# Optimization experiments

Measured on AMD Instinct MI355X. Metric: run time of the kernel, lower is better.

Reference implementation:

```python
import jax, jax.numpy as jnp
import numpy as np

N, E = 50000, 400000
FN, FE, FG = 32, 16, 16
H1, H2 = 256, 128


def seg_mean(x, idx, n):
    # mean of edge rows per segment; empty segments -> 0 (scatter_mean semantics)
    s = jax.ops.segment_sum(x, idx, num_segments=n)
    c = jax.ops.segment_sum(jnp.ones((x.shape[0], 1), x.dtype), idx, num_segments=n)
    return s / jnp.maximum(c, 1.0)


def setup_inputs() -> dict:
    key = jax.random.key(0)
    ks = jax.random.split(key, 32)
    g = lambda k, shape, s=0.05: jax.random.normal(k, shape, dtype=jnp.float32) * s
    return {
        'nodes': g(ks[0], (N, FN), 1.0),
        'edges': g(ks[1], (E, FE), 1.0),
        'globals_u': g(ks[2], (FG,), 1.0),
        'senders': jax.random.randint(ks[3], (E,), 0, N, dtype=jnp.int32),
        'receivers': jax.random.randint(ks[4], (E,), 0, N, dtype=jnp.int32),
        'We1': g(ks[5], (FE, H1)), 'be1': jnp.zeros((H1,), jnp.float32),
        'Wn1': g(ks[6], (FN, H1)), 'Win1': g(ks[7], (H1, H1)), 'Wout1': g(ks[8], (H1, H1)), 'bn1': jnp.zeros((H1,), jnp.float32),
        'Wu1': g(ks[9], (FG, H1)), 'Wgn1': g(ks[10], (H1, H1)), 'Wge1': g(ks[11], (H1, H1)), 'bu1': jnp.zeros((H1,), jnp.float32),
        'We2': g(ks[12], (H1, H2)), 'be2': jnp.zeros((H2,), jnp.float32),
        'Wn2': g(ks[13], (H1, H2)), 'Win2': g(ks[14], (H2, H2)), 'Wout2': g(ks[15], (H2, H2)), 'bn2': jnp.zeros((H2,), jnp.float32),
        'Wu2': g(ks[16], (H1, H2)), 'Wgn2': g(ks[17], (H2, H2)), 'Wge2': g(ks[18], (H2, H2)), 'bu2': jnp.zeros((H2,), jnp.float32),
    }


def reference(nodes, edges, globals_u, senders, receivers,
              We1, be1, Wn1, Win1, Wout1, bn1, Wu1, Wgn1, Wge1, bu1,
              We2, be2, Wn2, Win2, Wout2, bn2, Wu2, Wgn2, Wge2, bu2):
    n = nodes.shape[0]
    # --- block 1 (width 256) ---
    e1 = jax.nn.relu(edges @ We1 + be1)                                  # [E, H1]
    inc1 = seg_mean(e1, receivers, n)                                    # avg incoming edges per node
    out1 = seg_mean(e1, senders, n)                                      # avg outgoing edges per node
    n1 = jax.nn.relu(nodes @ Wn1 + inc1 @ Win1 + out1 @ Wout1 + bn1)     # [N, H1]
    u1 = jax.nn.relu(globals_u @ Wu1 + n1.mean(0) @ Wgn1 + e1.mean(0) @ Wge1 + bu1)  # [H1]
    # --- block 2 (width 128) ---
    e2 = jax.nn.relu(e1 @ We2 + be2)                                     # [E, H2]
    inc2 = seg_mean(e2, receivers, n)
    out2 = seg_mean(e2, senders, n)
    n2 = jax.nn.relu(n1 @ Wn2 + inc2 @ Win2 + out2 @ Wout2 + bn2)        # [N, H2]
    u2 = jax.nn.relu(u1 @ Wu2 + n2.mean(0) @ Wgn2 + e2.mean(0) @ Wge2 + bu2)  # [H2]
    return n2, e2, u2
```

## Files before the change

kernel.cpp:

```cpp
#include <hip/hip_runtime.h>
#include <hip/hip_bf16.h>
#include <stdint.h>

#define NN 50000
#define NE 400000
#define FN 32
#define FE 16
#define FG 16
#define H1 256
#define H2 128
#define M2 (2*NN)
#define SCAN_B 391
#define NPART 256

typedef unsigned short u16;
typedef __bf16 bfv8 __attribute__((ext_vector_type(8)));
typedef float f32v4 __attribute__((ext_vector_type(4)));
typedef u16 usv2 __attribute__((ext_vector_type(2)));
typedef u16 usv4 __attribute__((ext_vector_type(4)));
typedef u16 usv8 __attribute__((ext_vector_type(8)));

#define APK 264
#define AP2 136
#define EP1 40


__device__ __forceinline__ u16 f2b(float x){
  __hip_bfloat16 h = __float2bfloat16(x);
  return *reinterpret_cast<u16*>(&h);
}
__device__ __forceinline__ float bf2f(u16 u){
  union{uint32_t i; float f;} v; v.i = ((uint32_t)u) << 16; return v.f;
}

template<int NCK, int NNT, int PITCH>
__device__ __forceinline__ void gemm_tiles(const u16* a_s, const u16* __restrict__ pB,
                                           int w, int l, f32v4* acc)
{
  const int lr = l & 15, q = l >> 4;
  const bfv8* bp = (const bfv8*)pB;
  for (int ck = 0; ck < NCK; ck++){
    bfv8 a = *(const bfv8*)&a_s[(w*16 + lr)*PITCH + ck*32 + q*8];
    #pragma unroll
    for (int nt = 0; nt < NNT; nt++){
      bfv8 b = bp[(ck*NNT + nt)*64 + l];
      acc[nt] = __builtin_amdgcn_mfma_f32_16x16x32_bf16(a, b, acc[nt], 0, 0, 0);
    }
  }
}

template<int C4PR_LOG2>
__device__ __forceinline__ void stage_rows(u16* a_s, const float* __restrict__ src,
                                           long n0, int t)
{
  const int c4pr = 1 << C4PR_LOG2;
  for (int idx = t; idx < 64*c4pr; idx += 256){
    int row = idx >> C4PR_LOG2, c4 = idx & (c4pr - 1);
    long n = n0 + row;
    float x0=0.f, x1=0.f, x2=0.f, x3=0.f;
    if (n < NN){
      const float4 v = *(const float4*)&src[(n << (C4PR_LOG2 + 2)) + c4*4];
      x0 = v.x; x1 = v.y; x2 = v.z; x3 = v.w;
    }
    usv4 o; o.x = f2b(x0); o.y = f2b(x1); o.z = f2b(x2); o.w = f2b(x3);
    *(usv4*)&a_s[row*APK + c4*4] = o;
  }
}

struct PD { const float* src; u16* dst; int K, N, Ks, perm; };
struct PackArgs { PD d[8]; };

__global__ __launch_bounds__(64) void pack_weights(PackArgs A){
  int b = blockIdx.x, l = threadIdx.x;
  int mi = 0, base = 0;
  for (; mi < 8; mi++){
    int tiles = (A.d[mi].K >> 5) * (A.d[mi].N >> 4);
    if (b < base + tiles) break;
    base += tiles;
  }
  const PD d = A.d[mi];
  const int tile = b - base;
  const int ntn = d.N >> 4;
  const int ck = tile / ntn, nt = tile % ntn;
  const int lr = l & 15, q = l >> 4;
  const int col = nt*16 + lr;
  usv8 o;
  #pragma unroll
  for (int j = 0; j < 8; j++){
    int k = ck*32 + q*8 + j;
    int sk = (d.perm == 1) ? (((k & 15) << 4) | (k >> 4)) : k;
    o[j] = (k < d.Ks) ? f2b(d.src[(long)sk * d.N + col]) : (u16)0;
  }
  *(usv8*)&d.dst[((long)tile*64 + l)*8] = o;
}

__global__ __launch_bounds__(256) void csr_count(const int* __restrict__ recv,
    const int* __restrict__ send, int* cnt, int* pos_in, int* pos_out)
{
  int e = blockIdx.x*256 + threadIdx.x;
  if (e >= NE) return;
  pos_in [e] = atomicAdd(&cnt[recv[e]], 1);
  pos_out[e] = atomicAdd(&cnt[NN + send[e]], 1);
}

__global__ __launch_bounds__(256) void scan_blocks(const int* __restrict__ cnt,
    int* off, int* btot)
{
  __shared__ int s[256];
  int b = blockIdx.x, t = threadIdx.x;
  int i = b*256 + t;
  int v = (i < M2) ? cnt[i] : 0;
  s[t] = v; __syncthreads();
  int acc = v;
  for (int d = 1; d < 256; d <<= 1){
    int add = (t >= d) ? s[t-d] : 0;
    __syncthreads();
    acc += add; s[t] = acc;
    __syncthreads();
  }
  if (i < M2) off[i] = acc - v;
  if (t == 255) btot[b] = acc;
}

__global__ __launch_bounds__(256) void scan_tops(int* btot){
  __shared__ int s[512], ts[256];
  int t = threadIdx.x;
  s[t]     = (t < SCAN_B) ? btot[t] : 0;
  s[256+t] = (256+t < SCAN_B) ? btot[256+t] : 0;
  __syncthreads();
  int a0 = s[2*t], a1 = s[2*t+1];
  int tot = a0 + a1;
  ts[t] = tot; __syncthreads();
  int acc = tot;
  for (int d = 1; d < 256; d <<= 1){
    int add = (t >= d) ? ts[t-d] : 0;
    __syncthreads();
    acc += add; ts[t] = acc;
    __syncthreads();
  }
  int excl = acc - tot;
  if (2*t   < SCAN_B) btot[2*t]   = excl;
  if (2*t+1 < SCAN_B) btot[2*t+1] = excl + a0;
}

__global__ __launch_bounds__(256) void scan_fix(int* off, const int* __restrict__ btot){
  int i = blockIdx.x*256 + threadIdx.x;
  if (i < M2) off[i] += btot[blockIdx.x];
}

__global__ __launch_bounds__(256) void csr_fill(const int* __restrict__ recv,
    const int* __restrict__ send, const int* __restrict__ off,
    const int* __restrict__ pos_in, const int* __restrict__ pos_out, int* lis)
{
  int e = blockIdx.x*256 + threadIdx.x;
  if (e >= NE) return;
  lis[off[recv[e]]      + pos_in [e]] = e;
  lis[off[NN + send[e]] + pos_out[e]] = e;
}

__global__ __launch_bounds__(256) void edge1_kernel(const float* __restrict__ edges,
    const u16* __restrict__ pWe1, const float* __restrict__ be1,
    u16* __restrict__ e1b, float* __restrict__ e1p)
{
  __shared__ __align__(16) u16 a_es[64*EP1];
  __shared__ float cs_s[H1];
  __shared__ float bs[H1];
  const int t = threadIdx.x;
  const long e0 = (long)blockIdx.x * 64;
  const int w = t >> 6, l = t & 63, lr = l & 15, q = l >> 4;
  cs_s[t] = 0.f;
  bs[t] = be1[t];
  {
    int row = t >> 2, c4 = t & 3;
    float4 v = *(const float4*)&edges[(e0 + row)*FE + c4*4];
    usv4 o = { f2b(v.x), f2b(v.y), f2b(v.z), f2b(v.w) };
    *(usv4*)&a_es[row*EP1 + c4*4] = o;
    *(usv4*)&a_es[row*EP1 + 16 + c4*4] = (usv4){0,0,0,0};
  }
  __syncthreads();
  f32v4 acc[16];
  #pragma unroll
  for (int nt = 0; nt < 16; nt++) acc[nt] = (f32v4){0.f,0.f,0.f,0.f};
  gemm_tiles<1,16,EP1>(a_es, pWe1, w, l, acc);

  #pragma unroll
  for (int nt = 0; nt < 16; nt++){
    const float b = bs[nt*16 + lr];
    float part = 0.f;
    #pragma unroll
    for (int r = 0; r < 4; r++){
      float v = fmaxf(acc[nt][r] + b, 0.f);
      acc[nt][r] = v; part += v;
    }
    part += __shfl_xor(part, 16);
    part += __shfl_xor(part, 32);
    if (q == 0) atomicAdd(&cs_s[nt*16 + lr], part);
  }
  usv8 ob0[4], ob1[4];
  #pragma unroll
  for (int r = 0; r < 4; r++){
    #pragma unroll
    for (int h = 0; h < 8; h++){ ob0[r][h] = f2b(acc[h][r]); ob1[r][h] = f2b(acc[8+h][r]); }
  }
  __syncthreads();
  atomicAdd(&e1p[(blockIdx.x & (NPART-1))*H1 + t], cs_s[t]);
  #pragma unroll
  for (int r = 0; r < 4; r++){
    const int m = w*16 + q*4 + r;
    *(usv8*)&e1b[(e0 + m)*H1 + lr*16]     = ob0[r];
    *(usv8*)&e1b[(e0 + m)*H1 + lr*16 + 8] = ob1[r];
  }
}

__global__ __launch_bounds__(256) void e2_kernel(float* __restrict__ e2f,
    const u16* __restrict__ pWe2, const float* __restrict__ be2, float* __restrict__ e2p)
{
  __shared__ __align__(16) u16 a_s[64*APK];
  __shared__ float cs_s[H2];
  __shared__ float bs[H2];
  const int t = threadIdx.x;
  const long e0 = (long)blockIdx.x * 64;
  const int w = t >> 6, l = t & 63, lr = l & 15, q = l >> 4;
  if (t < H2){ cs_s[t] = 0.f; bs[t] = be2[t]; }
  const u16* e1u = (const u16*)e2f;
  for (int idx = t; idx < 64*32; idx += 256){
    int row = idx >> 5, ch = idx & 31;
    usv8 v = *(const usv8*)&e1u[(e0 + row)*H1 + ch*8];
    *(usv8*)&a_s[row*APK + ch*8] = v;
  }
  __syncthreads();
  f32v4 acc[8];
  #pragma unroll
  for (int nt = 0; nt < 8; nt++) acc[nt] = (f32v4){0.f,0.f,0.f,0.f};
  gemm_tiles<8,8,APK>(a_s, pWe2, w, l, acc);

  #pragma unroll
  for (int nt = 0; nt < 8; nt++){
    const float b = bs[nt*16 + lr];
    float part = 0.f;
    #pragma unroll
    for (int r = 0; r < 4; r++){
      float v = fmaxf(acc[nt][r] + b, 0.f);
      acc[nt][r] = v; part += v;
    }
    part += __shfl_xor(part, 16);
    part += __shfl_xor(part, 32);
    if (q == 0) atomicAdd(&cs_s[nt*16 + lr], part);
  }
  __syncthreads();
  float* fl = (float*)a_s;
  #pragma unroll
  for (int r = 0; r < 4; r++){
    const int m = w*16 + q*4 + r;
    const int sw = (m & 7) * 4;
    #pragma unroll
    for (int nt = 0; nt < 8; nt++)
      fl[m*128 + ((nt*16 + lr) ^ sw)] = acc[nt][r];
  }
  __syncthreads();
  if (t < H2) atomicAdd(&e2p[(blockIdx.x & (NPART-1))*H2 + t], cs_s[t]);
  {
    const int row = t >> 2, c = t & 3;
    const int sw = (row & 7) * 4;
    #pragma unroll
    for (int k = 0; k < 8; k++){
      const int wi = (c*32 + k*4) ^ sw;
      float4 v = *(const float4*)&fl[row*128 + wi];
      *(float4*)&e2f[(e0 + row)*H2 + c*32 + k*4] = v;
    }
  }
}

template<int PITCH>
__device__ __forceinline__ void gather_h1(u16* a_s, const u16* __restrict__ src,
    const int* roff, const int* __restrict__ lis, int w, int l)
{
  for (int rr = 0; rr < 16; rr++){
    int r = w + rr*4;
    int rs = roff[r], re = roff[r+1];
    float s0=0.f, s1=0.f, s2=0.f, s3=0.f;
    int j = rs;
    for (; j + 8 <= re; j += 8){
      int i0=lis[j],i1=lis[j+1],i2=lis[j+2],i3=lis[j+3];
      int i4=lis[j+4],i5=lis[j+5],i6=lis[j+6],i7=lis[j+7];
      usv4 a0 = *(const usv4*)&src[(long)i0*H1 + l*4];
      usv4 a1 = *(const usv4*)&src[(long)i1*H1 + l*4];
      usv4 a2 = *(const usv4*)&src[(long)i2*H1 + l*4];
      usv4 a3 = *(const usv4*)&src[(long)i3*H1 + l*4];
      usv4 a4 = *(const usv4*)&src[(long)i4*H1 + l*4];
      usv4 a5 = *(const usv4*)&src[(long)i5*H1 + l*4];
      usv4 a6 = *(const usv4*)&src[(long)i6*H1 + l*4];
      usv4 a7 = *(const usv4*)&src[(long)i7*H1 + l*4];
      s0 += ((bf2f(a0.x)+bf2f(a1.x)) + (bf2f(a2.x)+bf2f(a3.x)))
          + ((bf2f(a4.x)+bf2f(a5.x)) + (bf2f(a6.x)+bf2f(a7.x)));
      s1 += ((bf2f(a0.y)+bf2f(a1.y)) + (bf2f(a2.y)+bf2f(a3.y)))
          + ((bf2f(a4.y)+bf2f(a5.y)) + (bf2f(a6.y)+bf2f(a7.y)));
      s2 += ((bf2f(a0.z)+bf2f(a1.z)) + (bf2f(a2.z)+bf2f(a3.z)))
          + ((bf2f(a4.z)+bf2f(a5.z)) + (bf2f(a6.z)+bf2f(a7.z)));
      s3 += ((bf2f(a0.w)+bf2f(a1.w)) + (bf2f(a2.w)+bf2f(a3.w)))
          + ((bf2f(a4.w)+bf2f(a5.w)) + (bf2f(a6.w)+bf2f(a7.w)));
    }
    for (; j + 4 <= re; j += 4){
      int i0=lis[j],i1=lis[j+1],i2=lis[j+2],i3=lis[j+3];
      usv4 a0 = *(const usv4*)&src[(long)i0*H1 + l*4];
      usv4 a1 = *(const usv4*)&src[(long)i1*H1 + l*4];
      usv4 a2 = *(const usv4*)&src[(long)i2*H1 + l*4];
      usv4 a3 = *(const usv4*)&src[(long)i3*H1 + l*4];
      s0 += (bf2f(a0.x)+bf2f(a1.x)) + (bf2f(a2.x)+bf2f(a3.x));
      s1 += (bf2f(a0.y)+bf2f(a1.y)) + (bf2f(a2.y)+bf2f(a3.y));
      s2 += (bf2f(a0.z)+bf2f(a1.z)) + (bf2f(a2.z)+bf2f(a3.z));
      s3 += (bf2f(a0.w)+bf2f(a1.w)) + (bf2f(a2.w)+bf2f(a3.w));
    }
    for (; j < re; ++j){
      int i0 = lis[j];
      usv4 a0 = *(const usv4*)&src[(long)i0*H1 + l*4];
      s0 += bf2f(a0.x); s1 += bf2f(a0.y); s2 += bf2f(a0.z); s3 += bf2f(a0.w);
    }
    float rd = 1.f / fmaxf((float)(re - rs), 1.f);
    usv4 o = { f2b(s0*rd), f2b(s1*rd), f2b(s2*rd), f2b(s3*rd) };
    *(usv4*)&a_s[r*PITCH + l*4] = o;
  }
}

template<int PITCH>
__device__ __forceinline__ void gather_h2(u16* a_s, const float* __restrict__ src,
    const int* roff, const int* __restrict__ lis, int w, int l)
{
  for (int rr = 0; rr < 16; rr++){
    int r = w + rr*4;
    int rs = roff[r], re = roff[r+1];
    float s0=0.f, s1=0.f;
    int j = rs;
    for (; j + 8 <= re; j += 8){
      int i0=lis[j],i1=lis[j+1],i2=lis[j+2],i3=lis[j+3];
      int i4=lis[j+4],i5=lis[j+5],i6=lis[j+6],i7=lis[j+7];
      float2 a0 = *(const float2*)&src[(long)i0*H2 + l*2];
      float2 a1 = *(const float2*)&src[(long)i1*H2 + l*2];
      float2 a2 = *(const float2*)&src[(long)i2*H2 + l*2];
      float2 a3 = *(const float2*)&src[(long)i3*H2 + l*2];
      float2 a4 = *(const float2*)&src[(long)i4*H2 + l*2];
      float2 a5 = *(const float2*)&src[(long)i5*H2 + l*2];
      float2 a6 = *(const float2*)&src[(long)i6*H2 + l*2];
      float2 a7 = *(const float2*)&src[(long)i7*H2 + l*2];
      s0 += ((a0.x+a1.x) + (a2.x+a3.x)) + ((a4.x+a5.x) + (a6.x+a7.x));
      s1 += ((a0.y+a1.y) + (a2.y+a3.y)) + ((a4.y+a5.y) + (a6.y+a7.y));
    }
    for (; j + 4 <= re; j += 4){
      int i0=lis[j],i1=lis[j+1],i2=lis[j+2],i3=lis[j+3];
      float2 a0 = *(const float2*)&src[(long)i0*H2 + l*2];
      float2 a1 = *(const float2*)&src[(long)i1*H2 + l*2];
      float2 a2 = *(const float2*)&src[(long)i2*H2 + l*2];
      float2 a3 = *(const float2*)&src[(long)i3*H2 + l*2];
      s0 += (a0.x+a1.x) + (a2.x+a3.x);
      s1 += (a0.y+a1.y) + (a2.y+a3.y);
    }
    for (; j < re; ++j){
      int i0 = lis[j];
      float2 a0 = *(const float2*)&src[(long)i0*H2 + l*2];
      s0 += a0.x; s1 += a0.y;
    }
    float rd = 1.f / fmaxf((float)(re - rs), 1.f);
    usv2 o = { f2b(s0*rd), f2b(s1*rd) };
    *(usv2*)&a_s[r*PITCH + l*2] = o;
  }
}

__global__ __launch_bounds__(256, 4) void node1_kernel(
    const float* __restrict__ nodes, const u16* __restrict__ e1b,
    const int* __restrict__ off, const int* __restrict__ lis,
    const u16* __restrict__ pWn1, const u16* __restrict__ pWin1, const u16* __restrict__ pWout1,
    const float* __restrict__ bn1, u16* __restrict__ n1b, float* __restrict__ n1p)
{
  __shared__ __align__(16) u16 a_s[64*APK];
  __shared__ int roff[65], roff2[65];
  __shared__ float cs_s[H1];
  __shared__ float bs[H1];
  const int t = threadIdx.x;
  const long n0 = (long)blockIdx.x * 64;
  const int w = t >> 6, l = t & 63, lr = l & 15, q = l >> 4;

  cs_s[t] = 0.f;
  bs[t] = bn1[t];
  if (t <= 64){
    long idx = n0 + t;
    roff [t] = (idx >= NN) ? NE     : off[idx];
    roff2[t] = (idx >= NN) ? 2*NE   : off[NN + idx];
  }
  __syncthreads();

  f32v4 acc[16];
  #pragma unroll
  for (int nt = 0; nt < 16; nt++) acc[nt] = (f32v4){0.f,0.f,0.f,0.f};

  gather_h1<APK>(a_s, e1b, roff, lis, w, l);
  __syncthreads();
  gemm_tiles<8,16,APK>(a_s, pWin1, w, l, acc);
  __syncthreads();

  gather_h1<APK>(a_s, e1b, roff2, lis, w, l);
  __syncthreads();
  gemm_tiles<8,16,APK>(a_s, pWout1, w, l, acc);
  __syncthreads();

  stage_rows<3>(a_s, nodes, n0, t);
  __syncthreads();
  gemm_tiles<1,16,APK>(a_s, pWn1, w, l, acc);

  #pragma unroll
  for (int nt = 0; nt < 16; nt++){
    const float b = bs[nt*16 + lr];
    float part = 0.f;
    #pragma unroll
    for (int r = 0; r < 4; r++){
      const long n = n0 + w*16 + q*4 + r;
      float v = fmaxf(acc[nt][r] + b, 0.f);
      acc[nt][r] = v;
      if (n < NN) part += v;
    }
    part += __shfl_xor(part, 16);
    part += __shfl_xor(part, 32);
    if (q == 0) atomicAdd(&cs_s[nt*16 + lr], part);
  }
  __syncthreads();
  atomicAdd(&n1p[(blockIdx.x & (NPART-1))*H1 + t], cs_s[t]);
  #pragma unroll
  for (int r = 0; r < 4; r++){
    const int m = w*16 + q*4 + r;
    const long n = n0 + m;
    if (n < NN){
      usv8 o0, o1;
      #pragma unroll
      for (int h = 0; h < 8; h++){ o0[h] = f2b(acc[h][r]); o1[h] = f2b(acc[8+h][r]); }
      *(usv8*)&n1b[n*H1 + lr*16]     = o0;
      *(usv8*)&n1b[n*H1 + lr*16 + 8] = o1;
    }
  }
}

__global__ __launch_bounds__(256, 4) void node2_kernel(
    const u16* __restrict__ n1b, const float* __restrict__ e2f,
    const int* __restrict__ off, const int* __restrict__ lis,
    const u16* __restrict__ pWn2, const u16* __restrict__ pWin2, const u16* __restrict__ pWout2,
    const float* __restrict__ bn2, float* __restrict__ n2_out, float* __restrict__ n2p)
{
  __shared__ __align__(16) u16 a_s[64*AP2];
  __shared__ int roff[65], roff2[65];
  __shared__ float cs_s[H2];
  const int t = threadIdx.x;
  const long n0 = (long)blockIdx.x * 64;
  const int w = t >> 6, l = t & 63, lr = l & 15, q = l >> 4;

  if (t < H2) cs_s[t] = 0.f;
  if (t <= 64){
    long idx = n0 + t;
    roff [t] = (idx >= NN) ? NE     : off[idx];
    roff2[t] = (idx >= NN) ? 2*NE   : off[NN + idx];
  }
  __syncthreads();

  f32v4 acc[8];
  #pragma unroll
  for (int nt = 0; nt < 8; nt++) acc[nt] = (f32v4){0.f,0.f,0.f,0.f};

  for (int h = 0; h < 2; h++){
    for (int idx = t; idx < 64*16; idx += 256){
      int row = idx >> 4, ch = idx & 15;
      long n = n0 + row;
      usv8 v = (usv8){0,0,0,0,0,0,0,0};
      if (n < NN) v = *(const usv8*)&n1b[n*H1 + h*128 + ch*8];
      *(usv8*)&a_s[row*AP2 + ch*8] = v;
    }
    __syncthreads();
    gemm_tiles<4,8,AP2>(a_s, pWn2 + h*(4*8*64*8), w, l, acc);
    __syncthreads();
  }

  gather_h2<AP2>(a_s, e2f, roff, lis, w, l);
  __syncthreads();
  gemm_tiles<4,8,AP2>(a_s, pWin2, w, l, acc);
  __syncthreads();

  gather_h2<AP2>(a_s, e2f, roff2, lis, w, l);
  __syncthreads();
  gemm_tiles<4,8,AP2>(a_s, pWout2, w, l, acc);

  #pragma unroll
  for (int nt = 0; nt < 8; nt++){
    const float b = bn2[nt*16 + lr];
    float part = 0.f;
    #pragma unroll
    for (int r = 0; r < 4; r++){
      const long n = n0 + w*16 + q*4 + r;
      float v = fmaxf(acc[nt][r] + b, 0.f);
      acc[nt][r] = v;
      if (n < NN) part += v;
    }
    part += __shfl_xor(part, 16);
    part += __shfl_xor(part, 32);
    if (q == 0) atomicAdd(&cs_s[nt*16 + lr], part);
  }
  __syncthreads();
  if (t < H2) atomicAdd(&n2p[(blockIdx.x & (NPART-1))*H2 + t], cs_s[t]);
  #pragma unroll
  for (int nt = 0; nt < 8; nt++){
    const int j = nt*16 + lr;
    #pragma unroll
    for (int r = 0; r < 4; r++){
      const long n = n0 + w*16 + q*4 + r;
      if (n < NN) n2_out[n*H2 + j] = acc[nt][r];
    }
  }
}

__global__ void u1_kernel(const float* __restrict__ gu, const float* __restrict__ Wu1,
    const float* __restrict__ Wgn1, const float* __restrict__ Wge1, const float* __restrict__ bu1,
    const float* __restrict__ n1p, const float* __restrict__ e1p, float* __restrict__ u1v)
{
    __shared__ float ncs[H1], ecs[H1];
    const int j = threadIdx.x;
    float sn = 0.f, se = 0.f;
    #pragma unroll 8
    for (int c = 0; c < NPART; c++){ sn += n1p[c*H1 + j]; se += e1p[c*H1 + j]; }
    ncs[j] = sn; ecs[j] = se;
    __syncthreads();
    float acc = bu1[j];
    #pragma unroll
    for (int k = 0; k < FG; k++) acc += gu[k] * Wu1[k*H1 + j];
    for (int k = 0; k < H1; k++) acc += (ncs[k] * (1.f/NN)) * Wgn1[k*H1 + j];
    for (int k = 0; k < H1; k++) acc += (ecs[k] * (1.f/NE)) * Wge1[k*H1 + j];
    u1v[j] = fmaxf(acc, 0.f);
}

__global__ void u2_kernel(const float* __restrict__ u1v, const float* __restrict__ Wu2,
    const float* __restrict__ Wgn2, const float* __restrict__ Wge2, const float* __restrict__ bu2,
    const float* __restrict__ n2p, const float* __restrict__ e2p, float* __restrict__ u2_out)
{
    __shared__ float ncs[H2], ecs[H2];
    const int j = threadIdx.x;
    float sn = 0.f, se = 0.f;
    #pragma unroll 8
    for (int c = 0; c < NPART; c++){ sn += n2p[c*H2 + j]; se += e2p[c*H2 + j]; }
    ncs[j] = sn; ecs[j] = se;
    __syncthreads();
    float acc = bu2[j];
    for (int k = 0; k < H1; k++) acc += u1v[k] * Wu2[k*H2 + j];
    for (int k = 0; k < H2; k++) acc += (ncs[k] * (1.f/NN)) * Wgn2[k*H2 + j];
    for (int k = 0; k < H2; k++) acc += (ecs[k] * (1.f/NE)) * Wge2[k*H2 + j];
    u2_out[j] = fmaxf(acc, 0.f);
}

extern "C" void kernel_launch(void* const* d_in, const int* in_sizes, int n_in,
                              void* d_out, int out_size, void* d_ws, size_t ws_size,
                              hipStream_t stream)
{
    (void)in_sizes; (void)n_in; (void)out_size; (void)ws_size;
    const float* nodes = (const float*)d_in[0];
    const float* edges = (const float*)d_in[1];
    const float* gu    = (const float*)d_in[2];
    const int* senders   = (const int*)d_in[3];
    const int* receivers = (const int*)d_in[4];
    const float* We1  = (const float*)d_in[5];  const float* be1 = (const float*)d_in[6];
    const float* Wn1  = (const float*)d_in[7];  const float* Win1= (const float*)d_in[8];
    const float* Wout1= (const float*)d_in[9];  const float* bn1 = (const float*)d_in[10];
    const float* Wu1  = (const float*)d_in[11]; const float* Wgn1= (const float*)d_in[12];
    const float* Wge1 = (const float*)d_in[13]; const float* bu1 = (const float*)d_in[14];
    const float* We2  = (const float*)d_in[15]; const float* be2 = (const float*)d_in[16];
    const float* Wn2  = (const float*)d_in[17]; const float* Win2= (const float*)d_in[18];
    const float* Wout2= (const float*)d_in[19]; const float* bn2 = (const float*)d_in[20];
    const float* Wu2  = (const float*)d_in[21]; const float* Wgn2= (const float*)d_in[22];
    const float* Wge2 = (const float*)d_in[23]; const float* bu2 = (const float*)d_in[24];

    float* ws = (float*)d_ws;
    size_t o = 0;
    int*   cnt    = (int*)(ws + o);  o += M2;
    float* e1p    = ws + o;          o += (size_t)NPART*H1;
    float* n1p    = ws + o;          o += (size_t)NPART*H1;
    float* e2p    = ws + o;          o += (size_t)NPART*H2;
    float* n2p    = ws + o;          o += (size_t)NPART*H2;
    const size_t zero_bytes = o * sizeof(float);
    float* u1v    = ws + o;          o += 256;
    int*   off    = (int*)(ws + o);  o += M2;
    int*   pos_in = (int*)(ws + o);  o += NE;
    int*   pos_out= (int*)(ws + o);  o += NE;
    int*   lis    = (int*)(ws + o);  o += 2*NE;
    int*   btot   = (int*)(ws + o);  o += 400;

    u16* pbase = (u16*)(ws + o);
    size_t po = 0;
    u16* pWin1 = pbase + po;  po += (size_t)H1*H1;
    u16* pWout1= pbase + po;  po += (size_t)H1*H1;
    u16* pWn1  = pbase + po;  po += (size_t)FN*H1;
    u16* pWe1  = pbase + po;  po += (size_t)32*H1;
    u16* pWe2  = pbase + po;  po += (size_t)H1*H2;
    u16* pWn2  = pbase + po;  po += (size_t)H1*H2;
    u16* pWin2 = pbase + po;  po += (size_t)H2*H2;
    u16* pWout2= pbase + po;  po += (size_t)H2*H2;
    o += (po + 1) / 2;

    u16* n1b = (u16*)(ws + o);

    float* n2_out = (float*)d_out;
    float* e2f    = n2_out + (size_t)NN*H2;
    float* u2_out = n2_out + (size_t)(NN + NE)*H2;
    u16*   e1b    = (u16*)e2f;

    hipMemsetAsync(d_ws, 0, zero_bytes, stream);

    PackArgs pa;
    pa.d[0] = {Win1,  pWin1,  H1, H1, H1, 1};
    pa.d[1] = {Wout1, pWout1, H1, H1, H1, 1};
    pa.d[2] = {Wn1,   pWn1,   FN, H1, FN, 0};
    pa.d[3] = {We1,   pWe1,   32, H1, FE, 0};
    pa.d[4] = {We2,   pWe2,   H1, H2, H1, 1};
    pa.d[5] = {Wn2,   pWn2,   H1, H2, H1, 1};
    pa.d[6] = {Win2,  pWin2,  H2, H2, H2, 0};
    pa.d[7] = {Wout2, pWout2, H2, H2, H2, 0};
    int total_tiles = 0;
    for (int i = 0; i < 8; i++) total_tiles += (pa.d[i].K >> 5) * (pa.d[i].N >> 4);
    pack_weights<<<total_tiles, 64, 0, stream>>>(pa);

    const int EG = (NE + 255)/256;
    csr_count<<<EG, 256, 0, stream>>>(receivers, senders, cnt, pos_in, pos_out);
    scan_blocks<<<SCAN_B, 256, 0, stream>>>(cnt, off, btot);
    scan_tops<<<1, 256, 0, stream>>>(btot);
    scan_fix<<<SCAN_B, 256, 0, stream>>>(off, btot);
    csr_fill<<<EG, 256, 0, stream>>>(receivers, senders, off, pos_in, pos_out, lis);

    edge1_kernel<<<NE/64, 256, 0, stream>>>(edges, pWe1, be1, e1b, e1p);

    node1_kernel<<<(NN + 63)/64, 256, 0, stream>>>(nodes, e1b, off, lis,
        pWn1, pWin1, pWout1, bn1, n1b, n1p);

    u1_kernel<<<1, H1, 0, stream>>>(gu, Wu1, Wgn1, Wge1, bu1, n1p, e1p, u1v);

    e2_kernel<<<NE/64, 256, 0, stream>>>(e2f, pWe2, be2, e2p);

    node2_kernel<<<(NN + 63)/64, 256, 0, stream>>>(n1b, e2f, off, lis,
        pWn2, pWin2, pWout2, bn2, n2_out, n2p);

    u2_kernel<<<1, H2, 0, stream>>>(u1v, Wu2, Wgn2, Wge2, bu2, n2p, e2p, u2_out);
}
```

Before: 883.0 us.

## Halve node1 row tile and split output columns across warps for occupancy

node1_kernel now processes 32 nodes per block instead of 64. The four warps are arranged 2x2, each covering 16 rows by 8 output tiles, so the accumulator array shrinks from 16 to 8 MFMA tiles and the launch bound rises from 4 to 8 blocks per CU. The aim is more waves in flight to hide the latency of the irregular CSR gathers from e1b. In exchange, each block reads the packed weights for half as many rows, so weight traffic per node doubles, and there are twice as many blocks, each with its own atomic partial-sum update.

```diff
diff --git a/kernel.cpp b/kernel.cpp
--- a/kernel.cpp
+++ b/kernel.cpp
@@ -49,21 +49,19 @@
   }
 }
 
-template<int C4PR_LOG2>
-__device__ __forceinline__ void stage_rows(u16* a_s, const float* __restrict__ src,
-                                           long n0, int t)
-{
-  const int c4pr = 1 << C4PR_LOG2;
-  for (int idx = t; idx < 64*c4pr; idx += 256){
-    int row = idx >> C4PR_LOG2, c4 = idx & (c4pr - 1);
-    long n = n0 + row;
-    float x0=0.f, x1=0.f, x2=0.f, x3=0.f;
-    if (n < NN){
-      const float4 v = *(const float4*)&src[(n << (C4PR_LOG2 + 2)) + c4*4];
-      x0 = v.x; x1 = v.y; x2 = v.z; x3 = v.w;
-    }
-    usv4 o; o.x = f2b(x0); o.y = f2b(x1); o.z = f2b(x2); o.w = f2b(x3);
-    *(usv4*)&a_s[row*APK + c4*4] = o;
+template<int NCK, int NNT_TOT, int NNT, int PITCH>
+__device__ __forceinline__ void gemm_cs(const u16* a_s, const u16* __restrict__ pB,
+                                        int rbase, int ntb, int l, f32v4* acc)
+{
+  const int lr = l & 15, q = l >> 4;
+  const bfv8* bp = (const bfv8*)pB;
+  for (int ck = 0; ck < NCK; ck++){
+    bfv8 a = *(const bfv8*)&a_s[(rbase + lr)*PITCH + ck*32 + q*8];
+    #pragma unroll
+    for (int nt = 0; nt < NNT; nt++){
+      bfv8 b = bp[(ck*NNT_TOT + ntb + nt)*64 + l];
+      acc[nt] = __builtin_amdgcn_mfma_f32_16x16x32_bf16(a, b, acc[nt], 0, 0, 0);
+    }
   }
 }
 
@@ -271,11 +269,10 @@
   }
 }
 
-template<int PITCH>
-__device__ __forceinline__ void gather_h1(u16* a_s, const u16* __restrict__ src,
+__device__ __forceinline__ void gather_h1_32(u16* a_s, const u16* __restrict__ src,
     const int* roff, const int* __restrict__ lis, int w, int l)
 {
-  for (int rr = 0; rr < 16; rr++){
+  for (int rr = 0; rr < 8; rr++){
     int r = w + rr*4;
     int rs = roff[r], re = roff[r+1];
     float s0=0.f, s1=0.f, s2=0.f, s3=0.f;
@@ -318,7 +315,7 @@
     }
     float rd = 1.f / fmaxf((float)(re - rs), 1.f);
     usv4 o = { f2b(s0*rd), f2b(s1*rd), f2b(s2*rd), f2b(s3*rd) };
-    *(usv4*)&a_s[r*PITCH + l*4] = o;
+    *(usv4*)&a_s[r*APK + l*4] = o;
   }
 }
 
@@ -365,74 +362,85 @@
   }
 }
 
-__global__ __launch_bounds__(256, 4) void node1_kernel(
+__global__ __launch_bounds__(256, 8) void node1_kernel(
     const float* __restrict__ nodes, const u16* __restrict__ e1b,
     const int* __restrict__ off, const int* __restrict__ lis,
     const u16* __restrict__ pWn1, const u16* __restrict__ pWin1, const u16* __restrict__ pWout1,
     const float* __restrict__ bn1, u16* __restrict__ n1b, float* __restrict__ n1p)
 {
-  __shared__ __align__(16) u16 a_s[64*APK];
-  __shared__ int roff[65], roff2[65];
+  __shared__ __align__(16) u16 a_s[32*APK];
+  __shared__ int roff[33], roff2[33];
   __shared__ float cs_s[H1];
   __shared__ float bs[H1];
   const int t = threadIdx.x;
-  const long n0 = (long)blockIdx.x * 64;
+  const long n0 = (long)blockIdx.x * 32;
   const int w = t >> 6, l = t & 63, lr = l & 15, q = l >> 4;
+  const int rbase = (w & 1) * 16;
+  const int ntb   = (w >> 1) * 8;
 
   cs_s[t] = 0.f;
   bs[t] = bn1[t];
-  if (t <= 64){
+  if (t <= 32){
     long idx = n0 + t;
     roff [t] = (idx >= NN) ? NE     : off[idx];
     roff2[t] = (idx >= NN) ? 2*NE   : off[NN + idx];
   }
   __syncthreads();
 
-  f32v4 acc[16];
-  #pragma unroll
-  for (int nt = 0; nt < 16; nt++) acc[nt] = (f32v4){0.f,0.f,0.f,0.f};
-
-  gather_h1<APK>(a_s, e1b, roff, lis, w, l);
-  __syncthreads();
-  gemm_tiles<8,16,APK>(a_s, pWin1, w, l, acc);
-  __syncthreads();
-
-  gather_h1<APK>(a_s, e1b, roff2, lis, w, l);
-  __syncthreads();
-  gemm_tiles<8,16,APK>(a_s, pWout1, w, l, acc);
-  __syncthreads();
-
-  stage_rows<3>(a_s, nodes, n0, t);
-  __syncthreads();
-  gemm_tiles<1,16,APK>(a_s, pWn1, w, l, acc);
-
-  #pragma unroll
-  for (int nt = 0; nt < 16; nt++){
-    const float b = bs[nt*16 + lr];
+  f32v4 acc[8];
+  #pragma unroll
+  for (int nt = 0; nt < 8; nt++) acc[nt] = (f32v4){0.f,0.f,0.f,0.f};
+
+  gather_h1_32(a_s, e1b, roff, lis, w, l);
+  __syncthreads();
+  gemm_cs<8,16,8,APK>(a_s, pWin1, rbase, ntb, l, acc);
+  __syncthreads();
+
+  gather_h1_32(a_s, e1b, roff2, lis, w, l);
+  __syncthreads();
+  gemm_cs<8,16,8,APK>(a_s, pWout1, rbase, ntb, l, acc);
+  __syncthreads();
+
+  {
+    int row = t >> 3, c4 = t & 7;
+    long n = n0 + row;
+    float x0=0.f, x1=0.f, x2=0.f, x3=0.f;
+    if (n < NN){
+      const float4 v = *(const float4*)&nodes[n*FN + c4*4];
+      x0 = v.x; x1 = v.y; x2 = v.z; x3 = v.w;
+    }
+    usv4 o; o.x = f2b(x0); o.y = f2b(x1); o.z = f2b(x2); o.w = f2b(x3);
+    *(usv4*)&a_s[row*APK + c4*4] = o;
+  }
+  __syncthreads();
+  gemm_cs<1,16,8,APK>(a_s, pWn1, rbase, ntb, l, acc);
+
+  #pragma unroll
+  for (int nt = 0; nt < 8; nt++){
+    const float b = bs[(ntb + nt)*16 + lr];
     float part = 0.f;
     #pragma unroll
     for (int r = 0; r < 4; r++){
-      const long n = n0 + w*16 + q*4 + r;
+      const long n = n0 + rbase + q*4 + r;
       float v = fmaxf(acc[nt][r] + b, 0.f);
       acc[nt][r] = v;
       if (n < NN) part += v;
     }
     part += __shfl_xor(part, 16);
     part += __shfl_xor(part, 32);
-    if (q == 0) atomicAdd(&cs_s[nt*16 + lr], part);
+    if (q == 0) atomicAdd(&cs_s[(ntb + nt)*16 + lr], part);
   }
   __syncthreads();
   atomicAdd(&n1p[(blockIdx.x & (NPART-1))*H1 + t], cs_s[t]);
   #pragma unroll
   for (int r = 0; r < 4; r++){
-    const int m = w*16 + q*4 + r;
+    const int m = rbase + q*4 + r;
     const long n = n0 + m;
     if (n < NN){
-      usv8 o0, o1;
+      usv8 o0;
       #pragma unroll
-      for (int h = 0; h < 8; h++){ o0[h] = f2b(acc[h][r]); o1[h] = f2b(acc[8+h][r]); }
-      *(usv8*)&n1b[n*H1 + lr*16]     = o0;
-      *(usv8*)&n1b[n*H1 + lr*16 + 8] = o1;
+      for (int h = 0; h < 8; h++) o0[h] = f2b(acc[h][r]);
+      *(usv8*)&n1b[n*H1 + lr*16 + ntb] = o0;
     }
   }
 }
@@ -628,7 +636,7 @@
 
     edge1_kernel<<<NE/64, 256, 0, stream>>>(edges, pWe1, be1, e1b, e1p);
 
-    node1_kernel<<<(NN + 63)/64, 256, 0, stream>>>(nodes, e1b, off, lis,
+    node1_kernel<<<(NN + 31)/32, 256, 0, stream>>>(nodes, e1b, off, lis,
         pWn1, pWin1, pWout1, bn1, n1b, n1p);
 
     u1_kernel<<<1, H1, 0, stream>>>(gu, Wu1, Wgn1, Wge1, bu1, n1p, e1p, u1v);
```

Measured after the change: 1.035 ms. +17.2%, slower.

## Fuse both edge MLP layers into one kernel with e1 kept in workspace

Applied to the files above, without the earlier changes.

Adds an edge kernel that computes e1 = relu(edges@We1+b) and then immediately e2 = relu(e1@We2+b) from LDS. e1 now goes to a separate bf16 workspace buffer rather than aliasing the e2 output region. This removes the separate e2 pass that re-read e1 from global memory. It depends on workspace size being large enough, otherwise it falls back to the old path. It also needs more LDS per block, which may reduce occupancy.

```diff
diff --git a/kernel.cpp b/kernel.cpp
--- a/kernel.cpp
+++ b/kernel.cpp
@@ -156,6 +156,108 @@
   if (e >= NE) return;
   lis[off[recv[e]]      + pos_in [e]] = e;
   lis[off[NN + send[e]] + pos_out[e]] = e;
+}
+
+__global__ __launch_bounds__(256, 4) void edge_fused(const float* __restrict__ edges,
+    const u16* __restrict__ pWe1, const float* __restrict__ be1, float* __restrict__ e1p,
+    const u16* __restrict__ pWe2, const float* __restrict__ be2, float* __restrict__ e2p,
+    u16* __restrict__ e1b, float* __restrict__ e2f)
+{
+  __shared__ __align__(16) u16 a_s[64*APK];
+  __shared__ float cs1[H1], bs1[H1];
+  __shared__ float cs2[H2], bs2[H2];
+  const int t = threadIdx.x;
+  const long e0 = (long)blockIdx.x * 64;
+  const int w = t >> 6, l = t & 63, lr = l & 15, q = l >> 4;
+  cs1[t] = 0.f; bs1[t] = be1[t];
+  if (t < H2){ cs2[t] = 0.f; bs2[t] = be2[t]; }
+  {
+    int row = t >> 2, c4 = t & 3;
+    float4 v = *(const float4*)&edges[(e0 + row)*FE + c4*4];
+    usv4 o = { f2b(v.x), f2b(v.y), f2b(v.z), f2b(v.w) };
+    *(usv4*)&a_s[row*EP1 + c4*4] = o;
+    *(usv4*)&a_s[row*EP1 + 16 + c4*4] = (usv4){0,0,0,0};
+  }
+  __syncthreads();
+  f32v4 acc1[16];
+  #pragma unroll
+  for (int nt = 0; nt < 16; nt++) acc1[nt] = (f32v4){0.f,0.f,0.f,0.f};
+  gemm_tiles<1,16,EP1>(a_s, pWe1, w, l, acc1);
+
+  #pragma unroll
+  for (int nt = 0; nt < 16; nt++){
+    const float b = bs1[nt*16 + lr];
+    float part = 0.f;
+    #pragma unroll
+    for (int r = 0; r < 4; r++){
+      float v = fmaxf(acc1[nt][r] + b, 0.f);
+      acc1[nt][r] = v; part += v;
+    }
+    part += __shfl_xor(part, 16);
+    part += __shfl_xor(part, 32);
+    if (q == 0) atomicAdd(&cs1[nt*16 + lr], part);
+  }
+  usv8 ob0[4], ob1[4];
+  #pragma unroll
+  for (int r = 0; r < 4; r++){
+    #pragma unroll
+    for (int h = 0; h < 8; h++){ ob0[r][h] = f2b(acc1[h][r]); ob1[r][h] = f2b(acc1[8+h][r]); }
+  }
+  __syncthreads();
+  #pragma unroll
+  for (int r = 0; r < 4; r++){
+    const int m = w*16 + q*4 + r;
+    *(usv8*)&a_s[m*APK + lr*16]     = ob0[r];
+    *(usv8*)&a_s[m*APK + lr*16 + 8] = ob1[r];
+  }
+  __syncthreads();
+  f32v4 acc2[8];
+  #pragma unroll
+  for (int nt = 0; nt < 8; nt++) acc2[nt] = (f32v4){0.f,0.f,0.f,0.f};
+  gemm_tiles<8,8,APK>(a_s, pWe2, w, l, acc2);
+
+  #pragma unroll
+  for (int nt = 0; nt < 8; nt++){
+    const float b = bs2[nt*16 + lr];
+    float part = 0.f;
+    #pragma unroll
+    for (int r = 0; r < 4; r++){
+      float v = fmaxf(acc2[nt][r] + b, 0.f);
+      acc2[nt][r] = v; part += v;
+    }
+    part += __shfl_xor(part, 16);
+    part += __shfl_xor(part, 32);
+    if (q == 0) atomicAdd(&cs2[nt*16 + lr], part);
+  }
+  __syncthreads();
+  float* fl = (float*)a_s;
+  #pragma unroll
+  for (int r = 0; r < 4; r++){
+    const int m = w*16 + q*4 + r;
+    const int sw = (m & 7) * 4;
+    #pragma unroll
+    for (int nt = 0; nt < 8; nt++)
+      fl[m*128 + ((nt*16 + lr) ^ sw)] = acc2[nt][r];
+  }
+  __syncthreads();
+  atomicAdd(&e1p[(blockIdx.x & (NPART-1))*H1 + t], cs1[t]);
+  if (t < H2) atomicAdd(&e2p[(blockIdx.x & (NPART-1))*H2 + t], cs2[t]);
+  #pragma unroll
+  for (int r = 0; r < 4; r++){
+    const int m = w*16 + q*4 + r;
+    *(usv8*)&e1b[(e0 + m)*H1 + lr*16]     = ob0[r];
+    *(usv8*)&e1b[(e0 + m)*H1 + lr*16 + 8] = ob1[r];
+  }
+  {
+    const int row = t >> 2, c = t & 3;
+    const int sw = (row & 7) * 4;
+    #pragma unroll
+    for (int k = 0; k < 8; k++){
+      const int wi = (c*32 + k*4) ^ sw;
+      float4 v = *(const float4*)&fl[row*128 + wi];
+      *(float4*)&e2f[(e0 + row)*H2 + c*32 + k*4] = v;
+    }
+  }
 }
 
 __global__ __launch_bounds__(256) void edge1_kernel(const float* __restrict__ edges,
@@ -553,7 +655,7 @@
                               void* d_out, int out_size, void* d_ws, size_t ws_size,
                               hipStream_t stream)
 {
-    (void)in_sizes; (void)n_in; (void)out_size; (void)ws_size;
+    (void)in_sizes; (void)n_in; (void)out_size;
     const float* nodes = (const float*)d_in[0];
     const float* edges = (const float*)d_in[1];
     const float* gu    = (const float*)d_in[2];
@@ -598,11 +700,14 @@
     o += (po + 1) / 2;
 
     u16* n1b = (u16*)(ws + o);
+    o += (size_t)NN*H1/2;
+    u16* e1b_ws = (u16*)(ws + o);
+    const bool FUSE = ws_size >= (o + (size_t)NE*H1/2) * sizeof(float);
 
     float* n2_out = (float*)d_out;
     float* e2f    = n2_out + (size_t)NN*H2;
     float* u2_out = n2_out + (size_t)(NN + NE)*H2;
-    u16*   e1b    = (u16*)e2f;
+    u16*   e1b    = FUSE ? e1b_ws : (u16*)e2f;
 
     hipMemsetAsync(d_ws, 0, zero_bytes, stream);
 
@@ -626,17 +731,23 @@
     scan_fix<<<SCAN_B, 256, 0, stream>>>(off, btot);
     csr_fill<<<EG, 256, 0, stream>>>(receivers, senders, off, pos_in, pos_out, lis);
 
-    edge1_kernel<<<NE/64, 256, 0, stream>>>(edges, pWe1, be1, e1b, e1p);
-
-    node1_kernel<<<(NN + 63)/64, 256, 0, stream>>>(nodes, e1b, off, lis,
-        pWn1, pWin1, pWout1, bn1, n1b, n1p);
-
-    u1_kernel<<<1, H1, 0, stream>>>(gu, Wu1, Wgn1, Wge1, bu1, n1p, e1p, u1v);
-
-    e2_kernel<<<NE/64, 256, 0, stream>>>(e2f, pWe2, be2, e2p);
-
-    node2_kernel<<<(NN + 63)/64, 256, 0, stream>>>(n1b, e2f, off, lis,
-        pWn2, pWin2, pWout2, bn2, n2_out, n2p);
+    const int NG = (NN + 63)/64;
+    if (FUSE){
+      edge_fused<<<NE/64, 256, 0, stream>>>(edges, pWe1, be1, e1p, pWe2, be2, e2p, e1b, e2f);
+      node1_kernel<<<NG, 256, 0, stream>>>(nodes, e1b, off, lis,
+          pWn1, pWin1, pWout1, bn1, n1b, n1p);
+      u1_kernel<<<1, H1, 0, stream>>>(gu, Wu1, Wgn1, Wge1, bu1, n1p, e1p, u1v);
+      node2_kernel<<<NG, 256, 0, stream>>>(n1b, e2f, off, lis,
+          pWn2, pWin2, pWout2, bn2, n2_out, n2p);
+    } else {
+      edge1_kernel<<<NE/64, 256, 0, stream>>>(edges, pWe1, be1, e1b, e1p);
+      node1_kernel<<<NG, 256, 0, stream>>>(nodes, e1b, off, lis,
+          pWn1, pWin1, pWout1, bn1, n1b, n1p);
+      u1_kernel<<<1, H1, 0, stream>>>(gu, Wu1, Wgn1, Wge1, bu1, n1p, e1p, u1v);
+      e2_kernel<<<NE/64, 256, 0, stream>>>(e2f, pWe2, be2, e2p);
+      node2_kernel<<<NG, 256, 0, stream>>>(n1b, e2f, off, lis,
+          pWn2, pWin2, pWout2, bn2, n2_out, n2p);
+    }
 
     u2_kernel<<<1, H2, 0, stream>>>(u1v, Wu2, Wgn2, Wge2, bu2, n2p, e2p, u2_out);
 }
```

Measured after the change: 925.9 us. 4.9% more time.
